# Performance work log

Hardware: AMD Instinct MI355X
Metric: run time of the kernel (lower is better)

## Reference

```python
import jax, jax.numpy as jnp
import numpy as np

N, IN_DIM, HEADS, C = 100000, 128, 4, 32  # out_dim = HEADS*C = 128
E = 1600000


def setup_inputs() -> dict:
    key = jax.random.key(0)
    ks = jax.random.split(key, 9)
    x = jax.random.normal(ks[0], (N, IN_DIM), dtype=jnp.float32)
    edge_index = jax.random.randint(ks[1], (2, E), 0, N, dtype=jnp.int64)
    # GATConv params
    W = jax.random.normal(ks[2], (HEADS * C, IN_DIM), dtype=jnp.float32) * (1.0 / np.sqrt(IN_DIM))
    att_src = jax.random.normal(ks[3], (HEADS, C), dtype=jnp.float32) * 0.1
    att_dst = jax.random.normal(ks[4], (HEADS, C), dtype=jnp.float32) * 0.1
    bias = jax.random.normal(ks[5], (HEADS * C,), dtype=jnp.float32) * 0.01
    # complex phase + LayerNorm params
    phase = jax.random.normal(ks[6], (HEADS * C,), dtype=jnp.float32) * 0.02
    gamma = 1.0 + jax.random.normal(ks[7], (HEADS * C,), dtype=jnp.float32) * 0.01
    beta = jax.random.normal(ks[8], (HEADS * C,), dtype=jnp.float32) * 0.01
    return {"x": x, "edge_index": edge_index, "W": W, "att_src": att_src,
            "att_dst": att_dst, "bias": bias, "phase": phase, "gamma": gamma, "beta": beta}


def reference(x, edge_index, W, att_src, att_dst, bias, phase, gamma, beta):
    src, dst = edge_index[0], edge_index[1]
    h = (x @ W.T).reshape(N, HEADS, C)                      # [N,H,C]
    a_src = jnp.einsum('nhc,hc->nh', h, att_src)            # [N,H]
    a_dst = jnp.einsum('nhc,hc->nh', h, att_dst)
    e = jax.nn.leaky_relu(a_src[src] + a_dst[dst], 0.2)     # [E,H]
    # segment softmax over destination nodes (numerically stable)
    m = jax.ops.segment_max(e, dst, num_segments=N)         # [N,H]
    ex = jnp.exp(e - m[dst])
    s = jax.ops.segment_sum(ex, dst, num_segments=N)        # [N,H]
    alpha = ex / (s[dst] + 1e-16)                           # [E,H]
    msg = h[src] * alpha[:, :, None]                        # [E,H,C]
    out = jax.ops.segment_sum(msg, dst, num_segments=N).reshape(N, HEADS * C) + bias
    # complex phase magnitude: sqrt((h cos p)^2 + (h sin p)^2 + eps)
    mag = jnp.sqrt((out * jnp.cos(phase)) ** 2 + (out * jnp.sin(phase)) ** 2 + 1e-12)
    # LayerNorm
    mu = mag.mean(-1, keepdims=True)
    var = ((mag - mu) ** 2).mean(-1, keepdims=True)
    hn = (mag - mu) / jnp.sqrt(var + 1e-5) * gamma + beta
    return jax.nn.gelu(hn, approximate=False)
```

## Files before the change

kernel.cpp:

```cpp
#include <hip/hip_runtime.h>
#include <hip/hip_bf16.h>

#define N_ 100000
#define E_ 1600000
#define D_ 128
#define H_ 4
#define C_ 32
#define CAP 64
#define XSTR 136

using bf16 = __hip_bfloat16;
typedef __attribute__((ext_vector_type(8))) short short8;
typedef __attribute__((ext_vector_type(4))) float f32x4;
typedef __attribute__((ext_vector_type(2))) float f32x2;

__device__ __forceinline__ float u2f(unsigned u) { return __uint_as_float(u); }
__device__ __forceinline__ unsigned short f2bu(float v) {
  bf16 t = __float2bfloat16(v);
  return *(unsigned short*)&t;
}

__global__ __launch_bounds__(256) void k_build(const int* __restrict__ ei,
                                               int* __restrict__ cnt,
                                               int* __restrict__ slot) {
  const int e = blockIdx.x * 256 + threadIdx.x;
  if (e >= E_) return;
  const int d = ei[E_ + e];
  const int s = ei[e];
  const int pos = atomicAdd(&cnt[d], 1);
  if (pos < CAP) slot[d * CAP + pos] = s;
}

__global__ __launch_bounds__(256) void k_linear(
    const float* __restrict__ x, const float* __restrict__ W,
    const float* __restrict__ att_src, const float* __restrict__ att_dst,
    bf16* __restrict__ h, float* __restrict__ a_src, float* __restrict__ a_dst) {
  __shared__ unsigned short WB[16384];
  __shared__ unsigned short XS[64 * XSTR];
  __shared__ float ats[128], atd[128];
  const int tid = threadIdx.x;
  const int lane = tid & 63, w = tid >> 6;
  const int n15 = lane & 15, quad = lane >> 4;

  for (int i = tid; i < 16384; i += 256) {
    const int n = i >> 7, k = i & 127;
    const int kk = k >> 5, q = (k >> 3) & 3, j = k & 7;
    const int frag = kk * 8 + (n >> 4);
    WB[frag * 512 + q * 128 + (n & 15) * 8 + j] = f2bu(W[n * 128 + k]);
  }
  if (tid < 128) { ats[tid] = att_src[tid]; atd[tid] = att_dst[tid]; }
  __syncthreads();

  const int nrb = (N_ + 63) / 64;
  for (int rb = blockIdx.x; rb < nrb; rb += gridDim.x) {
    const int row0 = rb * 64;
    const int arow = row0 + w * 16 + n15;

    short8 af[4];
#pragma unroll
    for (int kk = 0; kk < 4; kk++) {
      float4 p = make_float4(0.f, 0.f, 0.f, 0.f);
      float4 q = make_float4(0.f, 0.f, 0.f, 0.f);
      if (arow < N_) {
        const float* xp = &x[(size_t)arow * 128 + kk * 32 + quad * 8];
        p = *(const float4*)xp;
        q = *(const float4*)(xp + 4);
      }
      short8 a;
      a[0] = f2bu(p.x); a[1] = f2bu(p.y); a[2] = f2bu(p.z); a[3] = f2bu(p.w);
      a[4] = f2bu(q.x); a[5] = f2bu(q.y); a[6] = f2bu(q.z); a[7] = f2bu(q.w);
      af[kk] = a;
    }

    f32x4 acc[8] = {};
#pragma unroll
    for (int kk = 0; kk < 4; kk++)
#pragma unroll
      for (int t = 0; t < 8; t++) {
        const short8 b = *(const short8*)&WB[(kk * 8 + t) * 512 + lane * 8];
        acc[t] = __builtin_amdgcn_mfma_f32_16x16x32_bf16(af[kk], b, acc[t], 0, 0, 0);
      }

#pragma unroll
    for (int t = 0; t < 8; t++)
#pragma unroll
      for (int reg = 0; reg < 4; reg++)
        XS[(w * 16 + quad * 4 + reg) * XSTR + t * 16 + n15] = f2bu(acc[t][reg]);

    const int lrow = lane >> 2, hd = lane & 3, cb = hd * 32;
    const int grow = row0 + w * 16 + lrow;
    if (grow < N_) {
      float ps = 0.f, pd = 0.f;
#pragma unroll
      for (int g = 0; g < 4; g++) {
        const uint4 v = *(const uint4*)&XS[(w * 16 + lrow) * XSTR + cb + g * 8];
        *(uint4*)&h[(size_t)grow * 128 + cb + g * 8] = v;
        const unsigned uu[4] = {v.x, v.y, v.z, v.w};
#pragma unroll
        for (int p2 = 0; p2 < 4; p2++) {
          const float f0 = u2f(uu[p2] << 16);
          const float f1 = u2f(uu[p2] & 0xffff0000u);
          const int cc = cb + g * 8 + p2 * 2;
          ps = fmaf(f0, ats[cc], ps);  ps = fmaf(f1, ats[cc + 1], ps);
          pd = fmaf(f0, atd[cc], pd);  pd = fmaf(f1, atd[cc + 1], pd);
        }
      }
      a_src[grow * 4 + hd] = ps;
      a_dst[grow * 4 + hd] = pd;
    }
  }
}

__global__ __launch_bounds__(256) void k_gather(
    const int* __restrict__ cnt, const int* __restrict__ slot,
    const float* __restrict__ a_src, const float* __restrict__ a_dst,
    const bf16* __restrict__ h, const float* __restrict__ bias,
    const float* __restrict__ gamma, const float* __restrict__ beta,
    float* __restrict__ out) {
  const int lane = threadIdx.x & 63;
  const int d = blockIdx.x * 4 + (threadIdx.x >> 6);
  if (d >= N_) return;
  const int head = lane >> 4;
  const int ch = lane * 2;
  const int deg0 = cnt[d];
  const int deg = deg0 < CAP ? deg0 : CAP;
  const float ad = a_dst[d * 4 + head];
  const int* __restrict__ srow = slot + (size_t)d * CAP;

  int my_src = 0;
  if (lane < deg) my_src = srow[lane];

  float acc0 = 0.f, acc1 = 0.f, sumw = 0.f;

  int j = 0;
  for (; j + 4 <= deg; j += 4) {
    const int s0 = __builtin_amdgcn_readlane(my_src, j);
    const int s1 = __builtin_amdgcn_readlane(my_src, j + 1);
    const int s2 = __builtin_amdgcn_readlane(my_src, j + 2);
    const int s3 = __builtin_amdgcn_readlane(my_src, j + 3);
    const float as0 = a_src[s0 * 4 + head];
    const float as1 = a_src[s1 * 4 + head];
    const float as2 = a_src[s2 * 4 + head];
    const float as3 = a_src[s3 * 4 + head];
    const unsigned h0 = *(const unsigned*)&h[((size_t)s0 << 7) + ch];
    const unsigned h1 = *(const unsigned*)&h[((size_t)s1 << 7) + ch];
    const unsigned h2 = *(const unsigned*)&h[((size_t)s2 << 7) + ch];
    const unsigned h3 = *(const unsigned*)&h[((size_t)s3 << 7) + ch];
    float e0 = as0 + ad; e0 = (e0 > 0.f) ? e0 : 0.2f * e0;
    float e1 = as1 + ad; e1 = (e1 > 0.f) ? e1 : 0.2f * e1;
    float e2 = as2 + ad; e2 = (e2 > 0.f) ? e2 : 0.2f * e2;
    float e3 = as3 + ad; e3 = (e3 > 0.f) ? e3 : 0.2f * e3;
    const float w0 = __expf(e0), w1 = __expf(e1);
    const float w2 = __expf(e2), w3 = __expf(e3);
    sumw += w0; sumw += w1; sumw += w2; sumw += w3;
    acc0 = fmaf(w0, u2f(h0 << 16), acc0); acc1 = fmaf(w0, u2f(h0 & 0xffff0000u), acc1);
    acc0 = fmaf(w1, u2f(h1 << 16), acc0); acc1 = fmaf(w1, u2f(h1 & 0xffff0000u), acc1);
    acc0 = fmaf(w2, u2f(h2 << 16), acc0); acc1 = fmaf(w2, u2f(h2 & 0xffff0000u), acc1);
    acc0 = fmaf(w3, u2f(h3 << 16), acc0); acc1 = fmaf(w3, u2f(h3 & 0xffff0000u), acc1);
  }
  for (; j < deg; ++j) {
    const int s = __builtin_amdgcn_readlane(my_src, j);
    const float as = a_src[s * 4 + head];
    const unsigned hv = *(const unsigned*)&h[((size_t)s << 7) + ch];
    float ev = as + ad;
    ev = (ev > 0.f) ? ev : 0.2f * ev;
    const float wv = __expf(ev);
    sumw += wv;
    acc0 = fmaf(wv, u2f(hv << 16), acc0);
    acc1 = fmaf(wv, u2f(hv & 0xffff0000u), acc1);
  }

  const float inv = 1.0f / (sumw + 1e-16f);
  const float2 bi = *(const float2*)&bias[ch];
  const float v0 = acc0 * inv + bi.x;
  const float v1 = acc1 * inv + bi.y;
  const float m0i = sqrtf(v0 * v0 + 1e-12f);
  const float m1i = sqrtf(v1 * v1 + 1e-12f);

  float s1r = m0i + m1i;
#pragma unroll
  for (int off = 32; off > 0; off >>= 1) s1r += __shfl_xor(s1r, off);
  const float mu = s1r * (1.0f / 128.0f);
  const float d0 = m0i - mu, d1 = m1i - mu;
  float q = d0 * d0 + d1 * d1;
#pragma unroll
  for (int off = 32; off > 0; off >>= 1) q += __shfl_xor(q, off);
  const float rstd = rsqrtf(q * (1.0f / 128.0f) + 1e-5f);
  const float2 ga = *(const float2*)&gamma[ch];
  const float2 be = *(const float2*)&beta[ch];
  const float hn0 = d0 * rstd * ga.x + be.x;
  const float hn1 = d1 * rstd * ga.y + be.y;
  const float g0 = 0.5f * hn0 * (1.0f + erff(hn0 * 0.70710678118654752f));
  const float g1 = 0.5f * hn1 * (1.0f + erff(hn1 * 0.70710678118654752f));
  f32x2 gv; gv.x = g0; gv.y = g1;
  __builtin_nontemporal_store(gv, (f32x2*)&out[(size_t)d * 128 + ch]);
}

extern "C" void kernel_launch(void* const* d_in, const int* in_sizes, int n_in,
                              void* d_out, int out_size, void* d_ws, size_t ws_size,
                              hipStream_t stream) {
  const float* x       = (const float*)d_in[0];
  const int*   ei      = (const int*)d_in[1];
  const float* W       = (const float*)d_in[2];
  const float* att_src = (const float*)d_in[3];
  const float* att_dst = (const float*)d_in[4];
  const float* bias    = (const float*)d_in[5];
  const float* gamma   = (const float*)d_in[7];
  const float* beta    = (const float*)d_in[8];
  float* out = (float*)d_out;

  bf16*  h     = (bf16*)d_ws;
  float* a_src = (float*)(h + (size_t)N_ * D_);
  float* a_dst = a_src + (size_t)N_ * H_;
  int*   cnt   = (int*)(a_dst + (size_t)N_ * H_);
  int*   slot  = cnt + (size_t)N_;

  (void)hipMemsetAsync(cnt, 0, (size_t)N_ * sizeof(int), stream);

  k_build<<<(E_ + 255) / 256, 256, 0, stream>>>(ei, cnt, slot);
  k_linear<<<768, 256, 0, stream>>>(x, W, att_src, att_dst, h, a_src, a_dst);
  k_gather<<<(N_ + 3) / 4, 256, 0, stream>>>(cnt, slot, a_src, a_dst, h,
                                             bias, gamma, beta, out);
}
```

Before: 346.6 us.

## Fuse CSR build and linear projection into one role-split kernel

Merges the edge-bucketing kernel and the MFMA linear kernel into a single launch where one third of the blocks do the atomic slot build and two thirds do the projection, so the memory/atomic-bound build overlaps with the compute-bound GEMM. Build blocks now process four edges per thread per iteration in a grid-stride loop, which adds memory-level parallelism. It also removes one kernel launch. The risk is load imbalance between the two roles and fewer linear blocks (512 instead of 768), with the build blocks paying for the large shared-memory allocation they never use, which lowers occupancy.

```diff
diff --git a/kernel.cpp b/kernel.cpp
--- a/kernel.cpp
+++ b/kernel.cpp
@@ -8,6 +8,8 @@
 #define C_ 32
 #define CAP 64
 #define XSTR 136
+#define NBUILD 256
+#define NLIN 512
 
 using bf16 = __hip_bfloat16;
 typedef __attribute__((ext_vector_type(8))) short short8;
@@ -20,25 +22,39 @@
   return *(unsigned short*)&t;
 }
 
-__global__ __launch_bounds__(256) void k_build(const int* __restrict__ ei,
-                                               int* __restrict__ cnt,
-                                               int* __restrict__ slot) {
-  const int e = blockIdx.x * 256 + threadIdx.x;
-  if (e >= E_) return;
-  const int d = ei[E_ + e];
-  const int s = ei[e];
-  const int pos = atomicAdd(&cnt[d], 1);
-  if (pos < CAP) slot[d * CAP + pos] = s;
-}
-
-__global__ __launch_bounds__(256) void k_linear(
+__global__ __launch_bounds__(256) void k_build_linear(
     const float* __restrict__ x, const float* __restrict__ W,
     const float* __restrict__ att_src, const float* __restrict__ att_dst,
+    const int* __restrict__ ei, int* __restrict__ cnt, int* __restrict__ slot,
     bf16* __restrict__ h, float* __restrict__ a_src, float* __restrict__ a_dst) {
   __shared__ unsigned short WB[16384];
   __shared__ unsigned short XS[64 * XSTR];
   __shared__ float ats[128], atd[128];
   const int tid = threadIdx.x;
+  const int bid = blockIdx.x;
+  const int role = bid % 3;
+
+  if (role == 0) {
+    const int bb = bid / 3;
+    for (int base = bb * 1024; base < E_; base += NBUILD * 1024) {
+      const int e0 = base + tid;
+      const int e1 = base + 256 + tid;
+      const int e2 = base + 512 + tid;
+      const int e3 = base + 768 + tid;
+      int d0 = 0, d1 = 0, d2 = 0, d3 = 0, s0 = 0, s1 = 0, s2 = 0, s3 = 0;
+      if (e0 < E_) { d0 = ei[E_ + e0]; s0 = ei[e0]; }
+      if (e1 < E_) { d1 = ei[E_ + e1]; s1 = ei[e1]; }
+      if (e2 < E_) { d2 = ei[E_ + e2]; s2 = ei[e2]; }
+      if (e3 < E_) { d3 = ei[E_ + e3]; s3 = ei[e3]; }
+      if (e0 < E_) { const int p = atomicAdd(&cnt[d0], 1); if (p < CAP) slot[d0 * CAP + p] = s0; }
+      if (e1 < E_) { const int p = atomicAdd(&cnt[d1], 1); if (p < CAP) slot[d1 * CAP + p] = s1; }
+      if (e2 < E_) { const int p = atomicAdd(&cnt[d2], 1); if (p < CAP) slot[d2 * CAP + p] = s2; }
+      if (e3 < E_) { const int p = atomicAdd(&cnt[d3], 1); if (p < CAP) slot[d3 * CAP + p] = s3; }
+    }
+    return;
+  }
+
+  const int lb = (bid / 3) * 2 + (role - 1);
   const int lane = tid & 63, w = tid >> 6;
   const int n15 = lane & 15, quad = lane >> 4;
 
@@ -52,7 +68,7 @@
   __syncthreads();
 
   const int nrb = (N_ + 63) / 64;
-  for (int rb = blockIdx.x; rb < nrb; rb += gridDim.x) {
+  for (int rb = lb; rb < nrb; rb += NLIN) {
     const int row0 = rb * 64;
     const int arow = row0 + w * 16 + n15;
 
@@ -217,8 +233,8 @@
 
   (void)hipMemsetAsync(cnt, 0, (size_t)N_ * sizeof(int), stream);
 
-  k_build<<<(E_ + 255) / 256, 256, 0, stream>>>(ei, cnt, slot);
-  k_linear<<<768, 256, 0, stream>>>(x, W, att_src, att_dst, h, a_src, a_dst);
+  k_build_linear<<<768, 256, 0, stream>>>(x, W, att_src, att_dst, ei, cnt,
+                                          slot, h, a_src, a_dst);
   k_gather<<<(N_ + 3) / 4, 256, 0, stream>>>(cnt, slot, a_src, a_dst, h,
                                              bias, gamma, beta, out);
 }
```

New measurement: 289.7 us. -16.4%, faster.
